# Kernel tuning notes

Hardware: AMD Instinct MI355X
Metric: run time of the kernel (lower is better)

The kernel has to match this reference:

```python
import jax, jax.numpy as jnp
import numpy as np

NP, NM = 50, 32          # pathways, misc tokens
T = NP + NM              # 82 total tokens
D = 24                   # token_dim for latent_dim=2048: (2048//82)//4*4
H, DH, FF = 4, 6, 96     # heads, head_dim, ffn dim (4*D)
B = 8192
EPS = 1e-5


def _ln(x, g, b):
    m = x.mean(-1, keepdims=True)
    v = ((x - m) ** 2).mean(-1, keepdims=True)
    return (x - m) / jnp.sqrt(v + EPS) * g + b


def _adapter(x, w1, b1, g1, bb1, w2, b2, g2, bb2, w3, b3):
    # Linear -> LN -> GELU -> (Dropout eval) -> Linear -> LN -> GELU -> Linear
    h = jax.nn.gelu(_ln(x @ w1.T + b1, g1, bb1), approximate=False)
    h = jax.nn.gelu(_ln(h @ w2.T + b2, g2, bb2), approximate=False)
    return h @ w3.T + b3


def _enc_layer(x, wqkv, bqkv, wo, bo, lg1, lb1, fw1, fb1, fw2, fb2, lg2, lb2):
    # post-norm TransformerEncoderLayer (PyTorch defaults: relu FFN, batch_first)
    Bx, Tx, Dx = x.shape
    qkv = x @ wqkv.T + bqkv                       # [B,T,3D]
    q, k, v = jnp.split(qkv, 3, axis=-1)
    sh = lambda a: a.reshape(Bx, Tx, H, DH).transpose(0, 2, 1, 3)
    q, k, v = sh(q), sh(k), sh(v)
    att = jax.nn.softmax(jnp.einsum('bhqd,bhkd->bhqk', q, k) / jnp.sqrt(jnp.float32(DH)), axis=-1)
    o = jnp.einsum('bhqk,bhkd->bhqd', att, v).transpose(0, 2, 1, 3).reshape(Bx, Tx, Dx)
    o = o @ wo.T + bo
    x = _ln(x + o, lg1, lb1)
    f = jax.nn.relu(x @ fw1.T + fb1) @ fw2.T + fb2
    return _ln(x + f, lg2, lb2)


def setup_inputs() -> dict:
    key = jax.random.key(0)
    ks = iter(jax.random.split(key, 40))
    r = lambda *s: jax.random.normal(next(ks), s, dtype=jnp.float32) * 0.02
    inp = {
        'gene': jax.random.normal(next(ks), (B, 5000), dtype=jnp.float32),
        'protein': jax.random.normal(next(ks), (B, 226), dtype=jnp.float32),
        'pathway_tokens': jax.random.normal(next(ks), (NP, D), dtype=jnp.float32),
        'misc_tokens': jax.random.normal(next(ks), (NM, D), dtype=jnp.float32),
        # gene adapter: 5000 -> 512 -> 256 -> 82
        'gw1': r(512, 5000), 'gb1': jnp.zeros(512), 'gg1': jnp.ones(512), 'gbb1': jnp.zeros(512),
        'gw2': r(256, 512), 'gb2': jnp.zeros(256), 'gg2': jnp.ones(256), 'gbb2': jnp.zeros(256),
        'gw3': r(T, 256), 'gb3': jnp.zeros(T),
        # protein adapter: 226 -> 512 -> 256 -> 82
        'pw1': r(512, 226), 'pb1': jnp.zeros(512), 'pg1': jnp.ones(512), 'pbb1': jnp.zeros(512),
        'pw2': r(256, 512), 'pb2': jnp.zeros(256), 'pg2': jnp.ones(256), 'pbb2': jnp.zeros(256),
        'pw3': r(T, 256), 'pb3': jnp.zeros(T),
        # token mixer: 2 stacked TransformerEncoder layers
        'wqkv': r(2, 3 * D, D), 'bqkv': jnp.zeros((2, 3 * D)),
        'wo': r(2, D, D), 'bo': jnp.zeros((2, D)),
        'lg1': jnp.ones((2, D)), 'lb1': jnp.zeros((2, D)),
        'fw1': r(2, FF, D), 'fb1': jnp.zeros((2, FF)),
        'fw2': r(2, D, FF), 'fb2': jnp.zeros((2, D)),
        'lg2': jnp.ones((2, D)), 'lb2': jnp.zeros((2, D)),
    }
    return inp


def reference(gene, protein, pathway_tokens, misc_tokens,
              gw1, gb1, gg1, gbb1, gw2, gb2, gg2, gbb2, gw3, gb3,
              pw1, pb1, pg1, pbb1, pw2, pb2, pg2, pbb2, pw3, pb3,
              wqkv, bqkv, wo, bo, lg1, lb1, fw1, fb1, fw2, fb2, lg2, lb2):
    all_tokens = jnp.concatenate([pathway_tokens, misc_tokens], axis=0)    # [T,D]
    gene_w = jax.nn.softmax(_adapter(gene, gw1, gb1, gg1, gbb1, gw2, gb2, gg2, gbb2, gw3, gb3), axis=-1)
    prot_w = jax.nn.softmax(_adapter(protein, pw1, pb1, pg1, pbb1, pw2, pb2, pg2, pbb2, pw3, pb3), axis=-1)
    # vectorized form of the per-batch loop: token_activations[b] += all_tokens * w[b,:,None]
    acts = (gene_w + prot_w)[:, :, None] * all_tokens[None]               # [B,T,D]
    for l in range(2):
        acts = _enc_layer(acts, wqkv[l], bqkv[l], wo[l], bo[l], lg1[l], lb1[l],
                          fw1[l], fb1[l], fw2[l], fb2[l], lg2[l], lb2[l])
    return acts
```

## Files before the change

kernel.cpp:

```cpp
#include <hip/hip_runtime.h>
#include <hip/hip_bf16.h>
#include <math.h>

typedef __attribute__((ext_vector_type(4))) float f32x4;
typedef __attribute__((ext_vector_type(8))) short s16x8;
typedef __attribute__((ext_vector_type(4))) short s16x4;
typedef __attribute__((ext_vector_type(4))) unsigned int u32x4;
typedef __attribute__((ext_vector_type(2))) unsigned int u32x2;
typedef _Float16 h2 __attribute__((ext_vector_type(2)));

static __device__ __forceinline__ unsigned short f2bf(float f) {
  unsigned int u = __builtin_bit_cast(unsigned int, f);
  u += 0x7FFFu + ((u >> 16) & 1u);
  return (unsigned short)(u >> 16);
}
static __device__ __forceinline__ unsigned int pk2bf(float a, float b) {
  return (unsigned int)f2bf(a) | ((unsigned int)f2bf(b) << 16);
}
static __device__ __forceinline__ float bf2f(unsigned short u) {
  return __builtin_bit_cast(float, (unsigned int)u << 16);
}
static __device__ __forceinline__ float gelu_exact(float x) {
  return 0.5f * x * (1.0f + erff(x * 0.7071067811865475f));
}
// ... 68 lines not shown
  __shared__ unsigned short Bs[8192];
  const int tid = threadIdx.x;
  const int lane = tid & 63;
  const int wid = tid >> 6;
  const int wm = wid >> 1, wn = wid & 1;
  const int lr = lane & 15;
  const int lkb = ((lane >> 4) & 3) * 16;
  const int l = blockIdx.x;
  const int xcd = l & 7;
  const int kl = l >> 3;
  const int nb = kl % NT;
  const int tm = (kl / NT) * 8 + xcd;
  const size_t abase = (size_t)tm * KT * 4096;
  const size_t bbase0 = (size_t)(2 * nb) * KT * 4096;
  const size_t bbase1 = (size_t)(2 * nb + 1) * KT * 4096;

  f32x4 acc[2][4];
  #pragma unroll
  for (int m = 0; m < 2; ++m)
    #pragma unroll
    for (int n = 0; n < 4; ++n) acc[m][n] = (f32x4){0.f,0.f,0.f,0.f};

  for (int tk = 0; tk < KT; ++tk) {
    __syncthreads();
    const unsigned short* at = At + abase + (size_t)tk * 4096;
    const unsigned short* b0 = Bt + bbase0 + (size_t)tk * 4096;
    const unsigned short* b1 = Bt + bbase1 + (size_t)tk * 4096;
    gll16(at + tid * 8,        (char*)As + tid * 16);
    gll16(at + 2048 + tid * 8, (char*)As + 4096 + tid * 16);
    gll16(b0 + tid * 8,        (char*)Bs + tid * 16);
    gll16(b0 + 2048 + tid * 8, (char*)Bs + 4096 + tid * 16);
    gll16(b1 + tid * 8,        (char*)Bs + 8192 + tid * 16);
    gll16(b1 + 2048 + tid * 8, (char*)Bs + 12288 + tid * 16);
    __syncthreads();
    #pragma unroll
    for (int kk = 0; kk < 2; ++kk) {
      const int kb = (kk * 64 + lkb) ^ ((lr & 7) << 4);
      s16x8 af[2], bfr[4];
      #pragma unroll
      for (int m = 0; m < 2; ++m) {
        const int r = wm * 32 + m * 16 + lr;
        af[m] = *(const s16x8*)((const char*)As + r * 128 + kb);
      }
      #pragma unroll
      for (int n = 0; n < 4; ++n) {
        const int cc = wn * 64 + n * 16 + lr;
        bfr[n] = *(const s16x8*)((const char*)Bs + (cc >> 6) * 8192 + (cc & 63) * 128 + kb);
      }
      #pragma unroll
      for (int m = 0; m < 2; ++m)
        #pragma unroll
        for (int n = 0; n < 4; ++n)
          acc[m][n] = __builtin_amdgcn_mfma_f32_16x16x32_bf16(af[m], bfr[n], acc[m][n], 0, 0, 0);
    }
  }
  const int crow = (lane >> 4) * 4;
  #pragma unroll
  for (int m = 0; m < 2; ++m) {
    const int row = tm * 64 + wm * 32 + m * 16 + crow;
    #pragma unroll
    for (int n = 0; n < 4; ++n) {
      const int col = nb * 128 + wn * 64 + n * 16 + lr;
      if (col < Ntrue) {
        const float bv = bias[col];
        #pragma unroll
        for (int i = 0; i < 4; ++i)
          C[(size_t)(row + i) * Nld + col] = acc[m][n][i] + bv;
      }
    }
  }
}

__global__ __launch_bounds__(256)
void ln_gelu_b16t_kernel(const float* __restrict__ X, const float* __restrict__ g,
                         const float* __restrict__ bta, unsigned short* __restrict__ Y,
                         int N, int TK) {
  const int lane = threadIdx.x & 63;
  const int row = blockIdx.x * 4 + (threadIdx.x >> 6);
  const int tmv = row >> 6, r = row & 63;
  const float* xr = X + (size_t)row * N;
  if (N == 512) {
    const int c0 = lane * 8;
    f32x4 a = *(const f32x4*)(xr + c0);
    f32x4 b = *(const f32x4*)(xr + c0 + 4);
    float s = a[0]+a[1]+a[2]+a[3]+b[0]+b[1]+b[2]+b[3];
    float ss = a[0]*a[0]+a[1]*a[1]+a[2]*a[2]+a[3]*a[3]+b[0]*b[0]+b[1]*b[1]+b[2]*b[2]+b[3]*b[3];
    #pragma unroll
    for (int off = 1; off < 64; off <<= 1) { s += __shfl_xor(s, off); ss += __shfl_xor(ss, off); }
    const float mean = s * (1.f/512.f);
    const float var = ss * (1.f/512.f) - mean * mean;
    const float rstd = rsqrtf(var + 1e-5f);
    float z[8];
    #pragma unroll
    for (int i = 0; i < 4; ++i) z[i]   = gelu_exact((a[i]-mean)*rstd*g[c0+i]   + bta[c0+i]);
    #pragma unroll
    for (int i = 0; i < 4; ++i) z[4+i] = gelu_exact((b[i]-mean)*rstd*g[c0+4+i] + bta[c0+4+i]);
    const int tk = lane >> 3, lcb = lane & 7;
    const size_t d16 = ((size_t)(tmv * TK + tk) << 9) + (r << 3) + (lcb ^ (r & 7));
    u32x4 o = { pk2bf(z[0],z[1]), pk2bf(z[2],z[3]), pk2bf(z[4],z[5]), pk2bf(z[6],z[7]) };
    *(u32x4*)(Y + d16 * 8) = o;
  } else {
    const int c0 = lane * 4;
    f32x4 a = *(const f32x4*)(xr + c0);
    float s = a[0]+a[1]+a[2]+a[3];
    float ss = a[0]*a[0]+a[1]*a[1]+a[2]*a[2]+a[3]*a[3];
    #pragma unroll
    for (int off = 1; off < 64; off <<= 1) { s += __shfl_xor(s, off); ss += __shfl_xor(ss, off); }
    const float mean = s * (1.f/256.f);
    const float var = ss * (1.f/256.f) - mean * mean;
    const float rstd = rsqrtf(var + 1e-5f);
    float z[4];
    #pragma unroll
    for (int i = 0; i < 4; ++i) z[i] = gelu_exact((a[i]-mean)*rstd*g[c0+i] + bta[c0+i]);
    const int tk = lane >> 4, lcb = (lane >> 1) & 7, half = lane & 1;
    const size_t d16 = ((size_t)(tmv * TK + tk) << 9) + (r << 3) + (lcb ^ (r & 7));
    u32x2 o = { pk2bf(z[0],z[1]), pk2bf(z[2],z[3]) };
    *(u32x2*)(Y + d16 * 8 + half * 4) = o;
  }
}

__global__ __launch_bounds__(256)
void softmax2_kernel(const float* __restrict__ la, const float* __restrict__ lp,
                     float* __restrict__ w, int B) {
  const int wid = threadIdx.x >> 6;
  const int lane = threadIdx.x & 63;
  const int row = blockIdx.x * 4 + wid;
  if (row >= B) return;
  const bool has2 = (lane < 18);
  const float* a = la + (size_t)row * 82;
  const float* p = lp + (size_t)row * 82;
  float a0 = a[lane], a1 = has2 ? a[64 + lane] : -1e30f;
  float m = fmaxf(a0, a1);
  #pragma unroll
  for (int off = 1; off < 64; off <<= 1) m = fmaxf(m, __shfl_xor(m, off));
  float ea0 = __expf(a0 - m);
  float ea1 = has2 ? __expf(a1 - m) : 0.f;
  float sa = ea0 + ea1;
  #pragma unroll
  for (int off = 1; off < 64; off <<= 1) sa += __shfl_xor(sa, off);
  float p0 = p[lane], p1 = has2 ? p[64 + lane] : -1e30f;
  float mp = fmaxf(p0, p1);
  #pragma unroll
  for (int off = 1; off < 64; off <<= 1) mp = fmaxf(mp, __shfl_xor(mp, off));
  float ep0 = __expf(p0 - mp);
  float ep1 = has2 ? __expf(p1 - mp) : 0.f;
  float sp = ep0 + ep1;
  #pragma unroll
  for (int off = 1; off < 64; off <<= 1) sp += __shfl_xor(sp, off);
  const float ia = 1.0f / sa, ip = 1.0f / sp;
  w[(size_t)row * 82 + lane] = ea0 * ia + ep0 * ip;
  if (has2) w[(size_t)row * 82 + 64 + lane] = ea1 * ia + ep1 * ip;
}

#define TSTR 40
#define VSTR 104
#define OFF_WQ 0
#define OFF_WO 6400
#define OFF_F1 8960
#define OFF_F2 16640
#define OFF_SA 23296
#define OFF_SP 38656
#define OFF_SV 54016
#define LDS_SHORTS 67328

static __device__ __forceinline__ s16x8 frag40(const unsigned short* buf, int rowBase, int lane) {
  const int r = rowBase + (lane & 15);
  return *(const s16x8*)(buf + r * TSTR + 8 * (lane >> 4));
}
static __device__ __forceinline__ s16x8 frag104(const unsigned short* buf, int rowBase, int kOff, int lane) {
  const int r = rowBase + (lane & 15);
  return *(const s16x8*)(buf + r * VSTR + kOff + 8 * (lane >> 4));
}

__global__ __launch_bounds__(256, 1)
void encoder_mfma_kernel(const float* __restrict__ w_sum,
                         const float* __restrict__ pathway, const float* __restrict__ misc,
                         const float* __restrict__ wqkv, const float* __restrict__ bqkv,
                         const float* __restrict__ wo, const float* __restrict__ bo,
                         const float* __restrict__ lg1, const float* __restrict__ lb1,
                         const float* __restrict__ fw1, const float* __restrict__ fb1,
                         const float* __restrict__ fw2, const float* __restrict__ fb2,
                         const float* __restrict__ lg2, const float* __restrict__ lb2,
                         float* __restrict__ out, int Btot) {
  extern __shared__ unsigned short lds[];
  const int tid = threadIdx.x;
  const int lane = tid & 63;
  const int wv = tid >> 6;
  const int g = lane >> 4;
  const int c = lane & 15;
  const int q4 = g * 4;

  #pragma unroll
  for (int l = 0; l < 2; ++l) {
    for (int r = tid; r < 80; r += 256) {
      unsigned short* dst = lds + OFF_WQ + l * 3200 + r * TSTR;
      unsigned int d[12];
      if (r < 72) {
        const float* s = wqkv + l * 1728 + r * 24;
        #pragma unroll
        for (int k = 0; k < 12; ++k) d[k] = pk2bf(s[2*k], s[2*k+1]);
      } else {
        #pragma unroll
        for (int k = 0; k < 12; ++k) d[k] = 0u;
      }
      *(u32x4*)(dst)      = (u32x4){d[0],d[1],d[2],d[3]};
      *(u32x4*)(dst + 8)  = (u32x4){d[4],d[5],d[6],d[7]};
      *(u32x4*)(dst + 16) = (u32x4){d[8],d[9],d[10],d[11]};
      *(u32x4*)(dst + 24) = (u32x4){0,0,0,0};
      *(u32x4*)(dst + 32) = (u32x4){0,0,0,0};
    }
    for (int r = tid; r < 32; r += 256) {
      unsigned short* dst = lds + OFF_WO + l * 1280 + r * TSTR;
      unsigned int d[12];
      if (r < 24) {
        const float* s = wo + l * 576 + r * 24;
        #pragma unroll
        for (int k = 0; k < 12; ++k) d[k] = pk2bf(s[2*k], s[2*k+1]);
      } else {
        #pragma unroll
        for (int k = 0; k < 12; ++k) d[k] = 0u;
      }
      *(u32x4*)(dst)      = (u32x4){d[0],d[1],d[2],d[3]};
      *(u32x4*)(dst + 8)  = (u32x4){d[4],d[5],d[6],d[7]};
      *(u32x4*)(dst + 16) = (u32x4){d[8],d[9],d[10],d[11]};
      *(u32x4*)(dst + 24) = (u32x4){0,0,0,0};
      *(u32x4*)(dst + 32) = (u32x4){0,0,0,0};
    }
    for (int r = tid; r < 96; r += 256) {
      unsigned short* dst = lds + OFF_F1 + l * 3840 + r * TSTR;
      const float* s = fw1 + l * 2304 + r * 24;
      unsigned int d[12];
      #pragma unroll
      for (int k = 0; k < 12; ++k) d[k] = pk2bf(s[2*k], s[2*k+1]);
      *(u32x4*)(dst)      = (u32x4){d[0],d[1],d[2],d[3]};
      *(u32x4*)(dst + 8)  = (u32x4){d[4],d[5],d[6],d[7]};
      *(u32x4*)(dst + 16) = (u32x4){d[8],d[9],d[10],d[11]};
      *(u32x4*)(dst + 24) = (u32x4){0,0,0,0};
      *(u32x4*)(dst + 32) = (u32x4){0,0,0,0};
    }
    for (int r = tid; r < 32; r += 256) {
      unsigned short* dst = lds + OFF_F2 + l * 3328 + r * VSTR;
      if (r < 24) {
        const float* s = fw2 + l * 2304 + r * 96;
        #pragma unroll
        for (int k4 = 0; k4 < 12; ++k4) {
          u32x4 d = { pk2bf(s[8*k4],   s[8*k4+1]), pk2bf(s[8*k4+2], s[8*k4+3]),
                      pk2bf(s[8*k4+4], s[8*k4+5]), pk2bf(s[8*k4+6], s[8*k4+7]) };
          *(u32x4*)(dst + 8*k4) = d;
        }
      } else {
        #pragma unroll
        for (int k4 = 0; k4 < 12; ++k4) *(u32x4*)(dst + 8*k4) = (u32x4){0,0,0,0};
      }
      *(u32x4*)(dst + 96) = (u32x4){0,0,0,0};
    }
  }
  __syncthreads();

  unsigned short* SA = lds + OFF_SA + wv * 3840;
  unsigned short* SP = lds + OFF_SP + wv * 3840;
  unsigned short* SV = lds + OFF_SV + wv * 3328;
  const int b = blockIdx.x * 4 + wv;
  const int bb = (b < Btot) ? b : (Btot - 1);

  for (int s = lane; s < 480; s += 64) ((u32x4*)SP)[s] = (u32x4){0,0,0,0};
  for (int s = lane; s < 416; s += 64) ((u32x4*)SV)[s] = (u32x4){0,0,0,0};
  for (int r = lane; r < 96; r += 64) {
    unsigned short* dst = SA + r * TSTR;
    if (r < 82) {
      const float* trow = (r < 50) ? (pathway + r * 24) : (misc + (r - 50) * 24);
      const float wvv = w_sum[(size_t)bb * 82 + r];
      unsigned int d[12];
      #pragma unroll
      for (int k = 0; k < 6; ++k) {
        f32x4 v = *(const f32x4*)(trow + 4 * k);
        d[2*k]   = pk2bf(wvv * v[0], wvv * v[1]);
        d[2*k+1] = pk2bf(wvv * v[2], wvv * v[3]);
      }
      *(u32x4*)(dst)      = (u32x4){d[0],d[1],d[2],d[3]};
      *(u32x4*)(dst + 8)  = (u32x4){d[4],d[5],d[6],d[7]};
      *(u32x4*)(dst + 16) = (u32x4){d[8],d[9],d[10],d[11]};
    } else {
      *(u32x4*)(dst)      = (u32x4){0,0,0,0};
      *(u32x4*)(dst + 8)  = (u32x4){0,0,0,0};
      *(u32x4*)(dst + 16) = (u32x4){0,0,0,0};
    }
    *(u32x4*)(dst + 24) = (u32x4){0,0,0,0};
    *(u32x4*)(dst + 32) = (u32x4){0,0,0,0};
  }

  float xres[6][2][4];
  #pragma unroll
  for (int m = 0; m < 6; ++m)
    #pragma unroll
    for (int n = 0; n < 2; ++n)
      #pragma unroll
      for (int i = 0; i < 4; ++i)
        xres[m][n][i] = bf2f(SA[(16*m + q4 + i) * TSTR + 16*n + c]);
  s16x8 af[6];
  #pragma unroll
  for (int m = 0; m < 6; ++m) af[m] = frag40(SA, 16*m, lane);

  const float QS = 0.5889777913f;
  const f32x4 Z4 = (f32x4){0.f, 0.f, 0.f, 0.f};

  #pragma unroll 1
  for (int l = 0; l < 2; ++l) {
    const unsigned short* Wq = lds + OFF_WQ + l * 3200;
    const unsigned short* Wo = lds + OFF_WO + l * 1280;
    const unsigned short* F1 = lds + OFF_F1 + l * 3840;
    const unsigned short* F2 = lds + OFF_F2 + l * 3328;
    const float* bqv = bqkv + l * 72;

    #pragma unroll
    for (int tn = 0; tn < 5; ++tn) {
      s16x8 bq = frag40(Wq, 16 * tn, lane);
      f32x4 a6[6];
      #pragma unroll
      for (int tm = 0; tm < 6; ++tm)
        a6[tm] = __builtin_amdgcn_mfma_f32_16x16x32_bf16(af[tm], bq, Z4, 0, 0, 0);
      const int j = tn * 16 + c;
      const float bj = (j < 72) ? bqv[j] : 0.f;
      #pragma unroll
      for (int tm = 0; tm < 6; ++tm) {
        const int tokb = 16 * tm + q4;
        if (j < 24) {
          #pragma unroll
          for (int i = 0; i < 4; ++i)
            SP[(tokb + i) * TSTR + j] = f2bf((a6[tm][i] + bj) * QS);
        } else if (j < 48) {
          #pragma unroll
          for (int i = 0; i < 4; ++i)
            SA[(tokb + i) * TSTR + (j - 24)] = f2bf(a6[tm][i] + bj);
        } else if (j < 72) {
          u32x2 w = { pk2bf(a6[tm][0] + bj, a6[tm][1] + bj),
                      pk2bf(a6[tm][2] + bj, a6[tm][3] + bj) };
          *(u32x2*)(SV + (j - 48) * VSTR + tokb) = w;
        }
      }
    }
    s16x8 qf[6];
    #pragma unroll
    for (int n = 0; n < 6; ++n) qf[n] = frag40(SP, 16*n, lane);

    f32x4 ot[2][6];
    #pragma unroll
    for (int m = 0; m < 2; ++m)
      #pragma unroll
      for (int n = 0; n < 6; ++n) ot[m][n] = Z4;
    float lsum[6] = {0.f, 0.f, 0.f, 0.f, 0.f, 0.f};
    #pragma unroll
    for (int p = 0; p < 3; ++p) {
      s16x8 ka0 = frag40(SA, 32*p, lane);
      s16x8 ka1 = frag40(SA, 32*p + 16, lane);
      f32x4 st[2][6];
      #pragma unroll
      for (int n = 0; n < 6; ++n) {
        st[0][n] = __builtin_amdgcn_mfma_f32_16x16x32_bf16(ka0, qf[n], Z4, 0, 0, 0);
        st[1][n] = __builtin_amdgcn_mfma_f32_16x16x32_bf16(ka1, qf[n], Z4, 0, 0, 0);
      }
      #pragma unroll
      for (int m = 0; m < 2; ++m)
        #pragma unroll
        for (int n = 0; n < 6; ++n) {
          const int kbase = 32*p + 16*m + q4;
          float pv[4];
          #pragma unroll
          for (int i = 0; i < 4; ++i) {
            const float e = exp2fast(st[m][n][i]);
            pv[i] = (kbase + i < 82) ? e : 0.f;
            lsum[n] += pv[i];
          }
          u32x2 w = { pk2bf(pv[0], pv[1]), pk2bf(pv[2], pv[3]) };
          *(u32x2*)(SP + (16*n + c) * TSTR + 16*m + q4) = w;
        }
      s16x8 va0 = frag104(SV, 0, 32*p, lane);
      s16x8 va1 = frag104(SV, 16, 32*p, lane);
      #pragma unroll
      for (int n = 0; n < 6; ++n) {
        s16x8 pf = frag40(SP, 16*n, lane);
        ot[0][n] = __builtin_amdgcn_mfma_f32_16x16x32_bf16(va0, pf, ot[0][n], 0, 0, 0);
        ot[1][n] = __builtin_amdgcn_mfma_f32_16x16x32_bf16(va1, pf, ot[1][n], 0, 0, 0);
      }
    }
    #pragma unroll
    for (int n = 0; n < 6; ++n) {
      float lt = lsum[n];
      lt += __shfl_xor(lt, 16);
      lt += __shfl_xor(lt, 32);
      const float inv = 1.0f / lt;
      #pragma unroll
      for (int m = 0; m < 2; ++m) {
        f32x4 o = ot[m][n];
        u32x2 w = { pk2bf(o[0]*inv, o[1]*inv), pk2bf(o[2]*inv, o[3]*inv) };
        *(u32x2*)(SP + (16*n + c) * TSTR + 16*m + q4) = w;
      }
    }
    s16x8 wof0 = frag40(Wo, 0, lane);
    s16x8 wof1 = frag40(Wo, 16, lane);
    const float bo0 = bo[l*24 + c];
    const float bo1 = (c < 8) ? bo[l*24 + 16 + c] : 0.f;
    const float g10 = lg1[l*24 + c];
    const float g11 = (c < 8) ? lg1[l*24 + 16 + c] : 0.f;
    const float be0 = lb1[l*24 + c];
    const float be1 = (c < 8) ? lb1[l*24 + 16 + c] : 0.f;
    float xn[6][2][4];
    #pragma unroll
    for (int m = 0; m < 6; ++m) {
      s16x8 oa = frag40(SP, 16*m, lane);
      f32x4 x0 = __builtin_amdgcn_mfma_f32_16x16x32_bf16(oa, wof0, Z4, 0, 0, 0);
      f32x4 x1 = __builtin_amdgcn_mfma_f32_16x16x32_bf16(oa, wof1, Z4, 0, 0, 0);
      #pragma unroll
      for (int i = 0; i < 4; ++i) {
        const float v0 = x0[i] + bo0 + xres[m][0][i];
        const float v1 = ((c < 8) ? (x1[i] + bo1) : 0.f) + xres[m][1][i];
        float s = v0 + v1;
        s += __shfl_xor(s, 1); s += __shfl_xor(s, 2);
        s += __shfl_xor(s, 4); s += __shfl_xor(s, 8);
        const float mu = s * (1.f / 24.f);
        const float d0 = v0 - mu;
        const float d1 = (c < 8) ? (v1 - mu) : 0.f;
        float vr = d0 * d0 + d1 * d1;
        vr += __shfl_xor(vr, 1); vr += __shfl_xor(vr, 2);
        vr += __shfl_xor(vr, 4); vr += __shfl_xor(vr, 8);
        const float rstd = rsqrtf(vr * (1.f / 24.f) + 1e-5f);
        xn[m][0][i] = d0 * rstd * g10 + be0;
        xn[m][1][i] = (c < 8) ? (d1 * rstd * g11 + be1) : 0.f;
      }
    }
    #pragma unroll
    for (int m = 0; m < 6; ++m)
      #pragma unroll
      for (int n = 0; n < 2; ++n)
        #pragma unroll
        for (int i = 0; i < 4; ++i)
          SP[(16*m + q4 + i) * TSTR + 16*n + c] = f2bf(xn[m][n][i]);
    s16x8 xnb[6];
    #pragma unroll
    for (int n = 0; n < 6; ++n) xnb[n] = frag40(SP, 16*n, lane);
    f32x4 ya[6][2];
    #pragma unroll
    for (int m = 0; m < 6; ++m) { ya[m][0] = Z4; ya[m][1] = Z4; }
    const float* fb1v = fb1 + l * 96;
    #pragma unroll
    for (int hp = 0; hp < 3; ++hp) {
      s16x8 f1a0 = frag40(F1, 32*hp, lane);
      s16x8 f1a1 = frag40(F1, 32*hp + 16, lane);
      #pragma unroll
      for (int n = 0; n < 6; ++n) {
        f32x4 h0 = __builtin_amdgcn_mfma_f32_16x16x32_bf16(f1a0, xnb[n], Z4, 0, 0, 0);
        f32x4 h1 = __builtin_amdgcn_mfma_f32_16x16x32_bf16(f1a1, xnb[n], Z4, 0, 0, 0);
        const int hb0 = 32*hp + q4, hb1 = 32*hp + 16 + q4;
        float r0[4], r1[4];
        #pragma unroll
        for (int i = 0; i < 4; ++i) {
          r0[i] = fmaxf(h0[i] + fb1v[hb0 + i], 0.f);
          r1[i] = fmaxf(h1[i] + fb1v[hb1 + i], 0.f);
        }
        u32x2 w0 = { pk2bf(r0[0], r0[1]), pk2bf(r0[2], r0[3]) };
        u32x2 w1 = { pk2bf(r1[0], r1[1]), pk2bf(r1[2], r1[3]) };
        *(u32x2*)(SA + (16*n + c) * TSTR + q4) = w0;
        *(u32x2*)(SA + (16*n + c) * TSTR + 16 + q4) = w1;
      }
      s16x8 f2f0 = frag104(F2, 0, 32*hp, lane);
      s16x8 f2f1 = frag104(F2, 16, 32*hp, lane);
      #pragma unroll
      for (int m = 0; m < 6; ++m) {
        s16x8 ha = frag40(SA, 16*m, lane);
        ya[m][0] = __builtin_amdgcn_mfma_f32_16x16x32_bf16(ha, f2f0, ya[m][0], 0, 0, 0);
        ya[m][1] = __builtin_amdgcn_mfma_f32_16x16x32_bf16(ha, f2f1, ya[m][1], 0, 0, 0);
      }
    }
    const float fb20 = fb2[l*24 + c];
    const float fb21 = (c < 8) ? fb2[l*24 + 16 + c] : 0.f;
    const float g20 = lg2[l*24 + c];
    const float g21 = (c < 8) ? lg2[l*24 + 16 + c] : 0.f;
    const float be20 = lb2[l*24 + c];
    const float be21 = (c < 8) ? lb2[l*24 + 16 + c] : 0.f;
    float xf[6][2][4];
    #pragma unroll
    for (int m = 0; m < 6; ++m)
      #pragma unroll
      for (int i = 0; i < 4; ++i) {
        const float v0 = ya[m][0][i] + fb20 + xn[m][0][i];
        const float v1 = ((c < 8) ? (ya[m][1][i] + fb21) : 0.f) + xn[m][1][i];
        float s = v0 + v1;
        s += __shfl_xor(s, 1); s += __shfl_xor(s, 2);
        s += __shfl_xor(s, 4); s += __shfl_xor(s, 8);
        const float mu = s * (1.f / 24.f);
        const float d0 = v0 - mu;
        const float d1 = (c < 8) ? (v1 - mu) : 0.f;
        float vr = d0 * d0 + d1 * d1;
        vr += __shfl_xor(vr, 1); vr += __shfl_xor(vr, 2);
        vr += __shfl_xor(vr, 4); vr += __shfl_xor(vr, 8);
        const float rstd = rsqrtf(vr * (1.f / 24.f) + 1e-5f);
        xf[m][0][i] = d0 * rstd * g20 + be20;
        xf[m][1][i] = (c < 8) ? (d1 * rstd * g21 + be21) : 0.f;
      }
    if (l == 0) {
      #pragma unroll
      for (int m = 0; m < 6; ++m)
        #pragma unroll
        for (int n = 0; n < 2; ++n)
          #pragma unroll
          for (int i = 0; i < 4; ++i) {
            SA[(16*m + q4 + i) * TSTR + 16*n + c] = f2bf(xf[m][n][i]);
            xres[m][n][i] = xf[m][n][i];
          }
      #pragma unroll
      for (int m = 0; m < 6; ++m) af[m] = frag40(SA, 16*m, lane);
    } else if (b < Btot) {
      #pragma unroll
      for (int m = 0; m < 6; ++m)
        #pragma unroll
        for (int i = 0; i < 4; ++i) {
          const int q = 16*m + q4 + i;
          if (q < 82) {
            out[(size_t)b * 1968 + q * 24 + c] = xf[m][0][i];
            if (c < 8) out[(size_t)b * 1968 + q * 24 + 16 + c] = xf[m][1][i];
          }
        }
    }
  }
}

#define GBM 64
#define GBN 128
#define GBK 64
#define GLDS 72

__global__ __launch_bounds__(256, 2)
void gemm_bias_kernel(const float* __restrict__ A, const float* __restrict__ Bw,
                      const float* __restrict__ bias, float* __restrict__ C,
                      int M, int N, int K) {
  __shared__ short As[GBM * GLDS];
  __shared__ short Bs[GBN * GLDS];
  const int tid = threadIdx.x;
  const int lane = tid & 63;
  const int wid = tid >> 6;
  const int wm = wid >> 1;
  const int wn = wid & 1;
  const int m0 = blockIdx.x * GBM;
  const int n0 = blockIdx.y * GBN;
  const int lr = lane & 15;
  const int lk = (lane >> 4) * 8;
  const bool kAligned = ((K & 3) == 0);
  f32x4 acc[2][4];
  #pragma unroll
  for (int i = 0; i < 2; ++i)
    #pragma unroll
    for (int j = 0; j < 4; ++j) acc[i][j] = (f32x4){0.f, 0.f, 0.f, 0.f};
  for (int k0 = 0; k0 < K; k0 += GBK) {
    __syncthreads();
    const bool fullK = kAligned && (k0 + GBK <= K);
    #pragma unroll
    for (int pass = 0; pass < 4; ++pass) {
      const int f = pass * 1024 + tid * 4;
      const int r = f >> 6, cc = f & 63;
      f32x4 v = (f32x4){0.f, 0.f, 0.f, 0.f};
      const float* src = A + (size_t)(m0 + r) * K + (k0 + cc);
      if (fullK) v = *(const f32x4*)src;
      else {
        #pragma unroll
        for (int i = 0; i < 4; ++i) if (k0 + cc + i < K) v[i] = src[i];
      }
      s16x4 sv = { (short)f2bf(v[0]), (short)f2bf(v[1]), (short)f2bf(v[2]), (short)f2bf(v[3]) };
      *(s16x4*)&As[r * GLDS + cc] = sv;
    }
    #pragma unroll
    for (int pass = 0; pass < 8; ++pass) {
      const int f = pass * 1024 + tid * 4;
      const int r = f >> 6, cc = f & 63;
      f32x4 v = (f32x4){0.f, 0.f, 0.f, 0.f};
      if (n0 + r < N) {
        const float* src = Bw + (size_t)(n0 + r) * K + (k0 + cc);
        if (fullK) v = *(const f32x4*)src;
        else {
          #pragma unroll
          for (int i = 0; i < 4; ++i) if (k0 + cc + i < K) v[i] = src[i];
        }
      }
      s16x4 sv = { (short)f2bf(v[0]), (short)f2bf(v[1]), (short)f2bf(v[2]), (short)f2bf(v[3]) };
      *(s16x4*)&Bs[r * GLDS + cc] = sv;
    }
    __syncthreads();
    #pragma unroll
    for (int kk = 0; kk < GBK; kk += 32) {
      s16x8 af2[2], bfr[4];
      #pragma unroll
      for (int m = 0; m < 2; ++m)
        af2[m] = *(const s16x8*)&As[(wm * 32 + m * 16 + lr) * GLDS + kk + lk];
      #pragma unroll
      for (int n = 0; n < 4; ++n)
        bfr[n] = *(const s16x8*)&Bs[(wn * 64 + n * 16 + lr) * GLDS + kk + lk];
      #pragma unroll
      for (int m = 0; m < 2; ++m)
        #pragma unroll
        for (int n = 0; n < 4; ++n)
          acc[m][n] = __builtin_amdgcn_mfma_f32_16x16x32_bf16(af2[m], bfr[n], acc[m][n], 0, 0, 0);
    }
  }
  const int crow = (lane >> 4) * 4;
  #pragma unroll
  for (int m = 0; m < 2; ++m) {
    const int row = m0 + wm * 32 + m * 16 + crow;
    #pragma unroll
    for (int n = 0; n < 4; ++n) {
      const int col = n0 + wn * 64 + n * 16 + lr;
      if (col < N) {
        const float bv = bias[col];
        #pragma unroll
        for (int i = 0; i < 4; ++i)
          C[(size_t)(row + i) * N + col] = acc[m][n][i] + bv;
      }
    }
  }
}

__global__ __launch_bounds__(256)
void ln_gelu_kernel(const float* __restrict__ X, const float* __restrict__ g,
                    const float* __restrict__ bta, float* __restrict__ Y, int N) {
  const int row = blockIdx.x;
  const float* xr = X + (size_t)row * N;
  float* yr = Y + (size_t)row * N;
  const int tid = threadIdx.x;
  const float e0 = xr[tid];
  float e1 = 0.f;
  const bool two = (N > 256);
  if (two) e1 = xr[tid + 256];
  float s = e0 + e1;
  float ss = e0 * e0 + e1 * e1;
  #pragma unroll
  for (int off = 1; off < 64; off <<= 1) { s += __shfl_xor(s, off); ss += __shfl_xor(ss, off); }
  __shared__ float red[8];
  const int w = tid >> 6;
  if ((tid & 63) == 0) { red[w] = s; red[4 + w] = ss; }
  __syncthreads();
  s  = red[0] + red[1] + red[2] + red[3];
  ss = red[4] + red[5] + red[6] + red[7];
  const float invN = 1.0f / (float)N;
  const float mean = s * invN;
  const float var = ss * invN - mean * mean;
  const float rstd = rsqrtf(var + 1e-5f);
  { const float z = (e0 - mean) * rstd * g[tid] + bta[tid]; yr[tid] = gelu_exact(z); }
  if (two) { const float z = (e1 - mean) * rstd * g[tid + 256] + bta[tid + 256]; yr[tid + 256] = gelu_exact(z); }
}

__global__ __launch_bounds__(256)
void pack_weights_kernel(const float* __restrict__ wqkv, const float* __restrict__ wo,
                         const float* __restrict__ fw1, const float* __restrict__ fw2,
                         unsigned int* __restrict__ dst) {
  const int i = blockIdx.x * 256 + threadIdx.x;
  if (i >= 6912) return;
  float a, b;
  if (i < 1728)      { a = wqkv[2 * i];            b = wqkv[2 * i + 1]; }
  else if (i < 2304) { int j = i - 1728; a = wo[2 * j];  b = wo[2 * j + 1]; }
  else if (i < 4608) { int j = i - 2304; a = fw1[2 * j]; b = fw1[2 * j + 1]; }
  else {
    int j = i - 4608; int layer = j / 1152; int r = j % 1152;
    int jp = r / 24; int d = r % 24;
    const float* s = fw2 + layer * 2304 + d * 96 + 2 * jp;
    a = s[0]; b = s[1];
  }
// ... 131 lines not shown
          acc_o[6*h+i] = dot2u(pp, vpu[6*h+i], acc_o[6*h+i]);
      }
    }
    #pragma unroll
    for (int h = 0; h < 4; ++h) {
      const float inv = 1.0f / lsum[h];
      #pragma unroll
      for (int dh = 0; dh < 6; ++dh) acc_o[6*h+dh] *= inv;
    }
    const float* BO = bo + layer * 24;
    h2 oh[12];
    #pragma unroll
    for (int i = 0; i < 12; ++i) oh[i] = pkh2(acc_o[2*i], acc_o[2*i+1]);
    float xo[24];
    #pragma unroll
    for (int j = 0; j < 24; ++j) {
      float s = BO[j];
      const unsigned int* wr = Woh + j * 12;
      #pragma unroll
      for (int kd = 0; kd < 12; ++kd) s = dot2u(oh[kd], wr[kd], s);
      xo[j] = x[j] + s;
    }
    float mean = 0.f;
    #pragma unroll
    for (int j = 0; j < 24; ++j) mean += xo[j];
    mean *= (1.f / 24.f);
    float var = 0.f;
    #pragma unroll
    for (int j = 0; j < 24; ++j) { const float dd = xo[j] - mean; var = fmaf(dd, dd, var); }
    var *= (1.f / 24.f);
    const float rstd = rsqrtf(var + 1e-5f);
    const float* G1 = lg1 + layer * 24;
    const float* Bl1 = lb1 + layer * 24;
    float xn[24];
    #pragma unroll
    for (int j = 0; j < 24; ++j) xn[j] = (xo[j] - mean) * rstd * G1[j] + Bl1[j];
    const float* Bf1 = fb1 + layer * 96;
    const float* Bf2 = fb2 + layer * 24;
    h2 xnh[12];
    #pragma unroll
    for (int i = 0; i < 12; ++i) xnh[i] = pkh2(xn[2*i], xn[2*i+1]);
    float y[24];
    #pragma unroll
    for (int d = 0; d < 24; ++d) y[d] = xn[d] + Bf2[d];
    #pragma unroll 1
    for (int jp = 0; jp < 48; ++jp) {
      float sa = Bf1[2*jp], sb = Bf1[2*jp+1];
      const unsigned int* w1 = F1h + (2*jp) * 12;
      #pragma unroll
      for (int kd = 0; kd < 12; ++kd) { sa = dot2u(xnh[kd], w1[kd], sa); sb = dot2u(xnh[kd], w1[12 + kd], sb); }
      sa = fmaxf(sa, 0.f);
      sb = fmaxf(sb, 0.f);
      h2 sp = pkh2(sa, sb);
      const unsigned int* w2 = F2t + jp * 24;
      #pragma unroll
      for (int d = 0; d < 24; ++d) y[d] = dot2u(sp, w2[d], y[d]);
    }
    float mean2 = 0.f;
    #pragma unroll
    for (int j = 0; j < 24; ++j) mean2 += y[j];
    mean2 *= (1.f / 24.f);
    float var2 = 0.f;
    #pragma unroll
    for (int j = 0; j < 24; ++j) { const float dd = y[j] - mean2; var2 = fmaf(dd, dd, var2); }
    var2 *= (1.f / 24.f);
    const float rstd2 = rsqrtf(var2 + 1e-5f);
    const float* G2 = lg2 + layer * 24;
    const float* Bl2 = lb2 + layer * 24;
    #pragma unroll
    for (int j = 0; j < 24; ++j) xf[j] = (y[j] - mean2) * rstd2 * G2[j] + Bl2[j];
    if (layer == 0) {
      #pragma unroll
      for (int j = 0; j < 24; ++j) x[j] = xf[j];
    }
    __syncthreads();
  }
  if (storeOK) {
    float* op = out + (size_t)b * 1968 + t * 24;
    #pragma unroll
    for (int d4 = 0; d4 < 6; ++d4) {
      f32x4 v = { xf[4*d4], xf[4*d4+1], xf[4*d4+2], xf[4*d4+3] };
      *(f32x4*)(op + 4 * d4) = v;
    }
  }
}

extern "C" void kernel_launch(void* const* d_in, const int* in_sizes, int n_in,
                              void* d_out, int out_size, void* d_ws, size_t ws_size,
                              hipStream_t stream) {
  const float* gene    = (const float*)d_in[0];
  const float* protein = (const float*)d_in[1];
  const float* pathway = (const float*)d_in[2];
  const float* misc    = (const float*)d_in[3];
  const float* gw1 = (const float*)d_in[4];
  const float* gb1 = (const float*)d_in[5];
  const float* gg1 = (const float*)d_in[6];
  const float* gbb1= (const float*)d_in[7];
  const float* gw2 = (const float*)d_in[8];
  const float* gb2 = (const float*)d_in[9];
  const float* gg2 = (const float*)d_in[10];
  const float* gbb2= (const float*)d_in[11];
  const float* gw3 = (const float*)d_in[12];
  const float* gb3 = (const float*)d_in[13];
  const float* pw1 = (const float*)d_in[14];
  const float* pb1 = (const float*)d_in[15];
  const float* pg1 = (const float*)d_in[16];
  const float* pbb1= (const float*)d_in[17];
  const float* pw2 = (const float*)d_in[18];
  const float* pb2 = (const float*)d_in[19];
  const float* pg2 = (const float*)d_in[20];
  const float* pbb2= (const float*)d_in[21];
  const float* pw3 = (const float*)d_in[22];
  const float* pb3 = (const float*)d_in[23];
  const float* wqkv= (const float*)d_in[24];
  const float* bqkv= (const float*)d_in[25];
  const float* wo  = (const float*)d_in[26];
  const float* bo  = (const float*)d_in[27];
  const float* lg1 = (const float*)d_in[28];
  const float* lb1 = (const float*)d_in[29];
  const float* fw1 = (const float*)d_in[30];
  const float* fb1 = (const float*)d_in[31];
  const float* fw2 = (const float*)d_in[32];
  const float* fb2 = (const float*)d_in[33];
  const float* lg2 = (const float*)d_in[34];
  const float* lb2 = (const float*)d_in[35];

  const int B = in_sizes[0] / 5000;
  dim3 blk(256);

  static int mfma_lds_ok = -1;
  if (mfma_lds_ok < 0) {
    hipError_t e = hipFuncSetAttribute((const void*)encoder_mfma_kernel,
        hipFuncAttributeMaxDynamicSharedMemorySize, LDS_SHORTS * 2);
    mfma_lds_ok = 1;
    (void)e;
  }

  size_t off = 0;
  auto take = [&](size_t bytes) { size_t r = off; off = (off + bytes + 255) & ~(size_t)255; return r; };
  const size_t o_geneB  = take((size_t)B * 5056 * 2);
  const size_t o_protB  = take((size_t)B * 256 * 2);
  const size_t o_gw1B   = take((size_t)512 * 5056 * 2);
  const size_t o_pw1B   = take((size_t)512 * 256 * 2);
  const size_t o_gw2B   = take((size_t)256 * 512 * 2);
  const size_t o_pw2B   = take((size_t)256 * 512 * 2);
  const size_t o_gw3B   = take((size_t)128 * 256 * 2);
  const size_t o_pw3B   = take((size_t)128 * 256 * 2);
  const size_t o_Cbuf   = take((size_t)B * 512 * 4);
  const size_t o_h1B    = take((size_t)B * 512 * 2);
  const size_t o_h2B    = take((size_t)B * 256 * 2);
  const size_t o_lg     = take((size_t)B * 82 * 4);
  const size_t o_lp     = take((size_t)B * 82 * 4);
  const size_t o_wsum   = take((size_t)B * 82 * 4);
  const size_t o_whb    = take((size_t)6912 * 4);
  const size_t need = off;

  if (need <= ws_size) {
    char* base = (char*)d_ws;
    unsigned short* geneB = (unsigned short*)(base + o_geneB);
    unsigned short* protB = (unsigned short*)(base + o_protB);
    unsigned short* gw1B  = (unsigned short*)(base + o_gw1B);
    unsigned short* pw1B  = (unsigned short*)(base + o_pw1B);
    unsigned short* gw2B  = (unsigned short*)(base + o_gw2B);
    unsigned short* pw2B  = (unsigned short*)(base + o_pw2B);
    unsigned short* gw3B  = (unsigned short*)(base + o_gw3B);
    unsigned short* pw3B  = (unsigned short*)(base + o_pw3B);
    float* Cbuf = (float*)(base + o_Cbuf);
    unsigned short* h1B = (unsigned short*)(base + o_h1B);
    unsigned short* h2B = (unsigned short*)(base + o_h2B);
    float* logits_g = (float*)(base + o_lg);
    float* logits_p = (float*)(base + o_lp);
    float* w_sum    = (float*)(base + o_wsum);

    const int MT = B / 64;
    {
      int t16 = MT * 79 * 512;
      convert_tile_kernel<<<dim3((t16 + 255) / 256), blk, 0, stream>>>(gene, geneB, B, 5000, 79, t16);
      t16 = MT * 4 * 512;
      convert_tile_kernel<<<dim3((t16 + 255) / 256), blk, 0, stream>>>(protein, protB, B, 226, 4, t16);
      t16 = 8 * 79 * 512;
      convert_tile_kernel<<<dim3((t16 + 255) / 256), blk, 0, stream>>>(gw1, gw1B, 512, 5000, 79, t16);
      t16 = 8 * 4 * 512;
      convert_tile_kernel<<<dim3((t16 + 255) / 256), blk, 0, stream>>>(pw1, pw1B, 512, 226, 4, t16);
      t16 = 4 * 8 * 512;
      convert_tile_kernel<<<dim3((t16 + 255) / 256), blk, 0, stream>>>(gw2, gw2B, 256, 512, 8, t16);
      convert_tile_kernel<<<dim3((t16 + 255) / 256), blk, 0, stream>>>(pw2, pw2B, 256, 512, 8, t16);
      t16 = 2 * 4 * 512;
      convert_tile_kernel<<<dim3((t16 + 255) / 256), blk, 0, stream>>>(gw3, gw3B, 82, 256, 4, t16);
      convert_tile_kernel<<<dim3((t16 + 255) / 256), blk, 0, stream>>>(pw3, pw3B, 82, 256, 4, t16);
    }
    gemm_bf16t_kernel<<<dim3(MT * 4), blk, 0, stream>>>(geneB, gw1B, gb1, Cbuf, 4, 79, 512, 512);
    ln_gelu_b16t_kernel<<<dim3(B / 4), blk, 0, stream>>>(Cbuf, gg1, gbb1, h1B, 512, 8);
    gemm_bf16t_kernel<<<dim3(MT * 2), blk, 0, stream>>>(h1B, gw2B, gb2, Cbuf, 2, 8, 256, 256);
    ln_gelu_b16t_kernel<<<dim3(B / 4), blk, 0, stream>>>(Cbuf, gg2, gbb2, h2B, 256, 4);
    gemm_bf16t_kernel<<<dim3(MT * 1), blk, 0, stream>>>(h2B, gw3B, gb3, logits_g, 1, 4, 82, 82);
    gemm_bf16t_kernel<<<dim3(MT * 4), blk, 0, stream>>>(protB, pw1B, pb1, Cbuf, 4, 4, 512, 512);
    ln_gelu_b16t_kernel<<<dim3(B / 4), blk, 0, stream>>>(Cbuf, pg1, pbb1, h1B, 512, 8);
    gemm_bf16t_kernel<<<dim3(MT * 2), blk, 0, stream>>>(h1B, pw2B, pb2, Cbuf, 2, 8, 256, 256);
    ln_gelu_b16t_kernel<<<dim3(B / 4), blk, 0, stream>>>(Cbuf, pg2, pbb2, h2B, 256, 4);
    gemm_bf16t_kernel<<<dim3(MT * 1), blk, 0, stream>>>(h2B, pw3B, pb3, logits_p, 1, 4, 82, 82);
    softmax2_kernel<<<dim3((B + 3) / 4), blk, 0, stream>>>(logits_g, logits_p, w_sum, B);
    encoder_mfma_kernel<<<dim3((B + 3) / 4), blk, LDS_SHORTS * 2, stream>>>(
        w_sum, pathway, misc, wqkv, bqkv, wo, bo, lg1, lb1,
        fw1, fb1, fw2, fb2, lg2, lb2, (float*)d_out, B);
    return;
  }

  float* bufA = (float*)d_ws;
  float* bufB = bufA + (size_t)B * 512;
  float* logits_g = bufB + (size_t)B * 512;
  float* logits_p = logits_g + (size_t)B * 82;
  float* w_sum    = logits_p + (size_t)B * 82;
  unsigned int* whb = (unsigned int*)(w_sum + (size_t)B * 82);

  pack_weights_kernel<<<dim3(27), blk, 0, stream>>>(wqkv, wo, fw1, fw2, whb);
  gemm_bias_kernel<<<dim3(B / 64, 4), blk, 0, stream>>>(gene, gw1, gb1, bufA, B, 512, 5000);
  ln_gelu_kernel<<<dim3(B), blk, 0, stream>>>(bufA, gg1, gbb1, bufB, 512);
  gemm_bias_kernel<<<dim3(B / 64, 2), blk, 0, stream>>>(bufB, gw2, gb2, bufA, B, 256, 512);
  ln_gelu_kernel<<<dim3(B), blk, 0, stream>>>(bufA, gg2, gbb2, bufB, 256);
  gemm_bias_kernel<<<dim3(B / 64, 1), blk, 0, stream>>>(bufB, gw3, gb3, logits_g, B, 82, 256);
  gemm_bias_kernel<<<dim3(B / 64, 4), blk, 0, stream>>>(protein, pw1, pb1, bufA, B, 512, 226);
  ln_gelu_kernel<<<dim3(B), blk, 0, stream>>>(bufA, pg1, pbb1, bufB, 512);
  gemm_bias_kernel<<<dim3(B / 64, 2), blk, 0, stream>>>(bufB, pw2, pb2, bufA, B, 256, 512);
  ln_gelu_kernel<<<dim3(B), blk, 0, stream>>>(bufA, pg2, pbb2, bufB, 256);
  gemm_bias_kernel<<<dim3(B / 64, 1), blk, 0, stream>>>(bufB, pw3, pb3, logits_p, B, 82, 256);
  softmax2_kernel<<<dim3((B + 3) / 4), blk, 0, stream>>>(logits_g, logits_p, w_sum, B);
  encoder_kernel<<<dim3((B + 2) / 3), blk, 0, stream>>>(w_sum, pathway, misc,
      whb, bqkv, bo, lg1, lb1, fb1, fb2, lg2, lb2, (float*)d_out, B);
}
```

Before: 613.6 us.

## Prepack encoder weights to bf16 in global memory and read fragments directly

Adds a small kernel that converts encoder weights to a padded bf16 layout in workspace once per call. The encoder kernel then loads MFMA weight fragments straight from global/L2 instead of having every block convert and stage them in LDS behind a barrier. Row strides shrink from 40/104 to 32/96, which cuts LDS to about 72KB and allows two blocks per CU via launch bounds. The cost is repeated global fragment loads of the weights and possible LDS bank conflicts from the unpadded power-of-two-ish strides.

```diff
diff --git a/kernel.cpp b/kernel.cpp
--- a/kernel.cpp
+++ b/kernel.cpp
@@ -244,34 +244,47 @@
   if (has2) w[(size_t)row * 82 + 64 + lane] = ea1 * ia + ep1 * ip;
 }
 
-#define TSTR 40
-#define VSTR 104
-#define OFF_WQ 0
-#define OFF_WO 6400
-#define OFF_F1 8960
-#define OFF_F2 16640
-#define OFF_SA 23296
-#define OFF_SP 38656
-#define OFF_SV 54016
-#define LDS_SHORTS 67328
-
-static __device__ __forceinline__ s16x8 frag40(const unsigned short* buf, int rowBase, int lane) {
-  const int r = rowBase + (lane & 15);
-  return *(const s16x8*)(buf + r * TSTR + 8 * (lane >> 4));
-}
-static __device__ __forceinline__ s16x8 frag104(const unsigned short* buf, int rowBase, int kOff, int lane) {
-  const int r = rowBase + (lane & 15);
-  return *(const s16x8*)(buf + r * VSTR + kOff + 8 * (lane >> 4));
-}
-
-__global__ __launch_bounds__(256, 1)
+__global__ __launch_bounds__(256)
+void pack_enc_kernel(const float* __restrict__ wqkv, const float* __restrict__ wo,
+                     const float* __restrict__ fw1, const float* __restrict__ fw2,
+                     unsigned short* __restrict__ dst) {
+  const int i = blockIdx.x * 256 + threadIdx.x;
+  if (i >= 19456) return;
+  float v = 0.f;
+  if (i < 5120) {
+    const int l = i / 2560, r = (i % 2560) >> 5, k = i & 31;
+    if (r < 72 && k < 24) v = wqkv[l * 1728 + r * 24 + k];
+  } else if (i < 7168) {
+    const int b2 = i - 5120; const int l = b2 / 1024, r = (b2 % 1024) >> 5, k = b2 & 31;
+    if (r < 24 && k < 24) v = wo[l * 576 + r * 24 + k];
+  } else if (i < 13312) {
+    const int b2 = i - 7168; const int l = b2 / 3072, r = (b2 % 3072) >> 5, k = b2 & 31;
+    if (k < 24) v = fw1[l * 2304 + r * 24 + k];
+  } else {
+    const int b2 = i - 13312; const int l = b2 / 3072, r = (b2 % 3072) / 96, h = b2 % 96;
+    if (r < 24) v = fw2[l * 2304 + r * 96 + h];
+  }
+  dst[i] = f2bf(v);
+}
+
+#define TSTR 32
+#define VSTR 96
+#define LDS_SHORTS 36864
+
+static __device__ __forceinline__ s16x8 frag32(const unsigned short* buf, int rowBase, int lane) {
+  return *(const s16x8*)(buf + (rowBase + (lane & 15)) * TSTR + 8 * (lane >> 4));
+}
+static __device__ __forceinline__ s16x8 frag96(const unsigned short* buf, int rowBase, int kOff, int lane) {
+  return *(const s16x8*)(buf + (rowBase + (lane & 15)) * VSTR + kOff + 8 * (lane >> 4));
+}
+
+__global__ __launch_bounds__(256, 2)
 void encoder_mfma_kernel(const float* __restrict__ w_sum,
                          const float* __restrict__ pathway, const float* __restrict__ misc,
-                         const float* __restrict__ wqkv, const float* __restrict__ bqkv,
-                         const float* __restrict__ wo, const float* __restrict__ bo,
+                         const unsigned short* __restrict__ wenc,
+                         const float* __restrict__ bqkv, const float* __restrict__ bo,
                          const float* __restrict__ lg1, const float* __restrict__ lb1,
-                         const float* __restrict__ fw1, const float* __restrict__ fb1,
-                         const float* __restrict__ fw2, const float* __restrict__ fb2,
+                         const float* __restrict__ fb1, const float* __restrict__ fb2,
                          const float* __restrict__ lg2, const float* __restrict__ lb2,
                          float* __restrict__ out, int Btot) {
   extern __shared__ unsigned short lds[];
@@ -282,81 +295,14 @@
   const int c = lane & 15;
   const int q4 = g * 4;
 
-  #pragma unroll
-  for (int l = 0; l < 2; ++l) {
-    for (int r = tid; r < 80; r += 256) {
-      unsigned short* dst = lds + OFF_WQ + l * 3200 + r * TSTR;
-      unsigned int d[12];
-      if (r < 72) {
-        const float* s = wqkv + l * 1728 + r * 24;
-        #pragma unroll
-        for (int k = 0; k < 12; ++k) d[k] = pk2bf(s[2*k], s[2*k+1]);
-      } else {
-        #pragma unroll
-        for (int k = 0; k < 12; ++k) d[k] = 0u;
-      }
-      *(u32x4*)(dst)      = (u32x4){d[0],d[1],d[2],d[3]};
-      *(u32x4*)(dst + 8)  = (u32x4){d[4],d[5],d[6],d[7]};
-      *(u32x4*)(dst + 16) = (u32x4){d[8],d[9],d[10],d[11]};
-      *(u32x4*)(dst + 24) = (u32x4){0,0,0,0};
-      *(u32x4*)(dst + 32) = (u32x4){0,0,0,0};
-    }
-    for (int r = tid; r < 32; r += 256) {
-      unsigned short* dst = lds + OFF_WO + l * 1280 + r * TSTR;
-      unsigned int d[12];
-      if (r < 24) {
-        const float* s = wo + l * 576 + r * 24;
-        #pragma unroll
-        for (int k = 0; k < 12; ++k) d[k] = pk2bf(s[2*k], s[2*k+1]);
-      } else {
-        #pragma unroll
-        for (int k = 0; k < 12; ++k) d[k] = 0u;
-      }
-      *(u32x4*)(dst)      = (u32x4){d[0],d[1],d[2],d[3]};
-      *(u32x4*)(dst + 8)  = (u32x4){d[4],d[5],d[6],d[7]};
-      *(u32x4*)(dst + 16) = (u32x4){d[8],d[9],d[10],d[11]};
-      *(u32x4*)(dst + 24) = (u32x4){0,0,0,0};
-      *(u32x4*)(dst + 32) = (u32x4){0,0,0,0};
-    }
-    for (int r = tid; r < 96; r += 256) {
-      unsigned short* dst = lds + OFF_F1 + l * 3840 + r * TSTR;
-      const float* s = fw1 + l * 2304 + r * 24;
-      unsigned int d[12];
-      #pragma unroll
-      for (int k = 0; k < 12; ++k) d[k] = pk2bf(s[2*k], s[2*k+1]);
-      *(u32x4*)(dst)      = (u32x4){d[0],d[1],d[2],d[3]};
-      *(u32x4*)(dst + 8)  = (u32x4){d[4],d[5],d[6],d[7]};
-      *(u32x4*)(dst + 16) = (u32x4){d[8],d[9],d[10],d[11]};
-      *(u32x4*)(dst + 24) = (u32x4){0,0,0,0};
-      *(u32x4*)(dst + 32) = (u32x4){0,0,0,0};
-    }
-    for (int r = tid; r < 32; r += 256) {
-      unsigned short* dst = lds + OFF_F2 + l * 3328 + r * VSTR;
-      if (r < 24) {
-        const float* s = fw2 + l * 2304 + r * 96;
-        #pragma unroll
-        for (int k4 = 0; k4 < 12; ++k4) {
-          u32x4 d = { pk2bf(s[8*k4],   s[8*k4+1]), pk2bf(s[8*k4+2], s[8*k4+3]),
-                      pk2bf(s[8*k4+4], s[8*k4+5]), pk2bf(s[8*k4+6], s[8*k4+7]) };
-          *(u32x4*)(dst + 8*k4) = d;
-        }
-      } else {
-        #pragma unroll
-        for (int k4 = 0; k4 < 12; ++k4) *(u32x4*)(dst + 8*k4) = (u32x4){0,0,0,0};
-      }
-      *(u32x4*)(dst + 96) = (u32x4){0,0,0,0};
-    }
-  }
-  __syncthreads();
-
-  unsigned short* SA = lds + OFF_SA + wv * 3840;
-  unsigned short* SP = lds + OFF_SP + wv * 3840;
-  unsigned short* SV = lds + OFF_SV + wv * 3328;
+  unsigned short* SA = lds + wv * 3072;
+  unsigned short* SP = lds + 12288 + wv * 3072;
+  unsigned short* SV = lds + 24576 + wv * 3072;
   const int b = blockIdx.x * 4 + wv;
   const int bb = (b < Btot) ? b : (Btot - 1);
 
-  for (int s = lane; s < 480; s += 64) ((u32x4*)SP)[s] = (u32x4){0,0,0,0};
-  for (int s = lane; s < 416; s += 64) ((u32x4*)SV)[s] = (u32x4){0,0,0,0};
+  for (int s = lane; s < 384; s += 64) ((u32x4*)SP)[s] = (u32x4){0,0,0,0};
+  for (int s = lane; s < 384; s += 64) ((u32x4*)SV)[s] = (u32x4){0,0,0,0};
   for (int r = lane; r < 96; r += 64) {
     unsigned short* dst = SA + r * TSTR;
     if (r < 82) {
@@ -378,7 +324,6 @@
       *(u32x4*)(dst + 16) = (u32x4){0,0,0,0};
     }
     *(u32x4*)(dst + 24) = (u32x4){0,0,0,0};
-    *(u32x4*)(dst + 32) = (u32x4){0,0,0,0};
   }
 
   float xres[6][2][4];
@@ -391,22 +336,22 @@
         xres[m][n][i] = bf2f(SA[(16*m + q4 + i) * TSTR + 16*n + c]);
   s16x8 af[6];
   #pragma unroll
-  for (int m = 0; m < 6; ++m) af[m] = frag40(SA, 16*m, lane);
+  for (int m = 0; m < 6; ++m) af[m] = frag32(SA, 16*m, lane);
 
   const float QS = 0.5889777913f;
   const f32x4 Z4 = (f32x4){0.f, 0.f, 0.f, 0.f};
 
   #pragma unroll 1
   for (int l = 0; l < 2; ++l) {
-    const unsigned short* Wq = lds + OFF_WQ + l * 3200;
-    const unsigned short* Wo = lds + OFF_WO + l * 1280;
-    const unsigned short* F1 = lds + OFF_F1 + l * 3840;
-    const unsigned short* F2 = lds + OFF_F2 + l * 3328;
+    const unsigned short* WQP = wenc + l * 2560;
+    const unsigned short* WOP = wenc + 5120 + l * 1024;
+    const unsigned short* F1P = wenc + 7168 + l * 3072;
+    const unsigned short* F2P = wenc + 13312 + l * 3072;
     const float* bqv = bqkv + l * 72;
 
     #pragma unroll
     for (int tn = 0; tn < 5; ++tn) {
-      s16x8 bq = frag40(Wq, 16 * tn, lane);
+      s16x8 bq = frag32(WQP, 16 * tn, lane);
       f32x4 a6[6];
       #pragma unroll
       for (int tm = 0; tm < 6; ++tm)
@@ -433,7 +378,7 @@
     }
     s16x8 qf[6];
     #pragma unroll
-    for (int n = 0; n < 6; ++n) qf[n] = frag40(SP, 16*n, lane);
+    for (int n = 0; n < 6; ++n) qf[n] = frag32(SP, 16*n, lane);
 
     f32x4 ot[2][6];
     #pragma unroll
@@ -443,8 +388,8 @@
     float lsum[6] = {0.f, 0.f, 0.f, 0.f, 0.f, 0.f};
     #pragma unroll
     for (int p = 0; p < 3; ++p) {
-      s16x8 ka0 = frag40(SA, 32*p, lane);
-      s16x8 ka1 = frag40(SA, 32*p + 16, lane);
+      s16x8 ka0 = frag32(SA, 32*p, lane);
+      s16x8 ka1 = frag32(SA, 32*p + 16, lane);
       f32x4 st[2][6];
       #pragma unroll
       for (int n = 0; n < 6; ++n) {
@@ -466,11 +411,11 @@
           u32x2 w = { pk2bf(pv[0], pv[1]), pk2bf(pv[2], pv[3]) };
           *(u32x2*)(SP + (16*n + c) * TSTR + 16*m + q4) = w;
         }
-      s16x8 va0 = frag104(SV, 0, 32*p, lane);
-      s16x8 va1 = frag104(SV, 16, 32*p, lane);
+      s16x8 va0 = frag96(SV, 0, 32*p, lane);
+      s16x8 va1 = frag96(SV, 16, 32*p, lane);
       #pragma unroll
       for (int n = 0; n < 6; ++n) {
-        s16x8 pf = frag40(SP, 16*n, lane);
+        s16x8 pf = frag32(SP, 16*n, lane);
         ot[0][n] = __builtin_amdgcn_mfma_f32_16x16x32_bf16(va0, pf, ot[0][n], 0, 0, 0);
         ot[1][n] = __builtin_amdgcn_mfma_f32_16x16x32_bf16(va1, pf, ot[1][n], 0, 0, 0);
       }
@@ -488,8 +433,8 @@
         *(u32x2*)(SP + (16*n + c) * TSTR + 16*m + q4) = w;
       }
     }
-    s16x8 wof0 = frag40(Wo, 0, lane);
-    s16x8 wof1 = frag40(Wo, 16, lane);
+    s16x8 wof0 = frag32(WOP, 0, lane);
+    s16x8 wof1 = frag32(WOP, 16, lane);
     const float bo0 = bo[l*24 + c];
     const float bo1 = (c < 8) ? bo[l*24 + 16 + c] : 0.f;
     const float g10 = lg1[l*24 + c];
@@ -499,7 +444,7 @@
     float xn[6][2][4];
     #pragma unroll
     for (int m = 0; m < 6; ++m) {
-      s16x8 oa = frag40(SP, 16*m, lane);
+      s16x8 oa = frag32(SP, 16*m, lane);
       f32x4 x0 = __builtin_amdgcn_mfma_f32_16x16x32_bf16(oa, wof0, Z4, 0, 0, 0);
       f32x4 x1 = __builtin_amdgcn_mfma_f32_16x16x32_bf16(oa, wof1, Z4, 0, 0, 0);
       #pragma unroll
@@ -529,15 +474,15 @@
           SP[(16*m + q4 + i) * TSTR + 16*n + c] = f2bf(xn[m][n][i]);
     s16x8 xnb[6];
     #pragma unroll
-    for (int n = 0; n < 6; ++n) xnb[n] = frag40(SP, 16*n, lane);
+    for (int n = 0; n < 6; ++n) xnb[n] = frag32(SP, 16*n, lane);
     f32x4 ya[6][2];
     #pragma unroll
     for (int m = 0; m < 6; ++m) { ya[m][0] = Z4; ya[m][1] = Z4; }
     const float* fb1v = fb1 + l * 96;
     #pragma unroll
     for (int hp = 0; hp < 3; ++hp) {
-      s16x8 f1a0 = frag40(F1, 32*hp, lane);
-      s16x8 f1a1 = frag40(F1, 32*hp + 16, lane);
+      s16x8 f1a0 = frag32(F1P, 32*hp, lane);
+      s16x8 f1a1 = frag32(F1P, 32*hp + 16, lane);
       #pragma unroll
       for (int n = 0; n < 6; ++n) {
         f32x4 h0 = __builtin_amdgcn_mfma_f32_16x16x32_bf16(f1a0, xnb[n], Z4, 0, 0, 0);
@@ -554,11 +499,11 @@
         *(u32x2*)(SA + (16*n + c) * TSTR + q4) = w0;
         *(u32x2*)(SA + (16*n + c) * TSTR + 16 + q4) = w1;
       }
-      s16x8 f2f0 = frag104(F2, 0, 32*hp, lane);
-      s16x8 f2f1 = frag104(F2, 16, 32*hp, lane);
+      s16x8 f2f0 = frag96(F2P, 0, 32*hp, lane);
+      s16x8 f2f1 = frag96(F2P, 16, 32*hp, lane);
       #pragma unroll
       for (int m = 0; m < 6; ++m) {
-        s16x8 ha = frag40(SA, 16*m, lane);
+        s16x8 ha = frag32(SA, 16*m, lane);
         ya[m][0] = __builtin_amdgcn_mfma_f32_16x16x32_bf16(ha, f2f0, ya[m][0], 0, 0, 0);
         ya[m][1] = __builtin_amdgcn_mfma_f32_16x16x32_bf16(ha, f2f1, ya[m][1], 0, 0, 0);
       }
@@ -600,7 +545,7 @@
             xres[m][n][i] = xf[m][n][i];
           }
       #pragma unroll
-      for (int m = 0; m < 6; ++m) af[m] = frag40(SA, 16*m, lane);
+      for (int m = 0; m < 6; ++m) af[m] = frag32(SA, 16*m, lane);
     } else if (b < Btot) {
       #pragma unroll
       for (int m = 0; m < 6; ++m)
@@ -1038,7 +983,7 @@
   const size_t o_lg     = take((size_t)B * 82 * 4);
   const size_t o_lp     = take((size_t)B * 82 * 4);
   const size_t o_wsum   = take((size_t)B * 82 * 4);
-  const size_t o_whb    = take((size_t)6912 * 4);
+  const size_t o_wenc   = take((size_t)19456 * 2);
   const size_t need = off;
 
   if (need <= ws_size) {
@@ -1057,8 +1002,10 @@
     float* logits_g = (float*)(base + o_lg);
     float* logits_p = (float*)(base + o_lp);
     float* w_sum    = (float*)(base + o_wsum);
+    unsigned short* wenc = (unsigned short*)(base + o_wenc);
 
     const int MT = B / 64;
+    pack_enc_kernel<<<dim3(76), blk, 0, stream>>>(wqkv, wo, fw1, fw2, wenc);
     {
       int t16 = MT * 79 * 512;
       convert_tile_kernel<<<dim3((t16 + 255) / 256), blk, 0, stream>>>(gene, geneB, B, 5000, 79, t16);
@@ -1087,8 +1034,8 @@
     gemm_bf16t_kernel<<<dim3(MT * 1), blk, 0, stream>>>(h2B, pw3B, pb3, logits_p, 1, 4, 82, 82);
     softmax2_kernel<<<dim3((B + 3) / 4), blk, 0, stream>>>(logits_g, logits_p, w_sum, B);
     encoder_mfma_kernel<<<dim3((B + 3) / 4), blk, LDS_SHORTS * 2, stream>>>(
-        w_sum, pathway, misc, wqkv, bqkv, wo, bo, lg1, lb1,
-        fw1, fb1, fw2, fb2, lg2, lb2, (float*)d_out, B);
+        w_sum, pathway, misc, wenc, bqkv, bo, lg1, lb1,
+        fb1, fb2, lg2, lb2, (float*)d_out, B);
     return;
   }
 
```

Result: slower. 630.8 us (+2.8%).
